# Kernel optimization log

Measured on AMD Instinct MI355X. Metric: run time of the kernel, lower is better.

## Reference

```python
import jax, jax.numpy as jnp
import numpy as np

B, S, D, H = 2, 2048, 2048, 32
HD = D // H  # head_dim = 64
NEG = -1e10


def setup_inputs() -> dict:
    key = jax.random.key(0)
    k1, k2, k3 = jax.random.split(key, 3)
    hidden_states = jax.random.normal(k1, (B, S, D), dtype=jnp.float32)
    W = jax.random.normal(k2, (D, 3 * D), dtype=jnp.float32) * (1.0 / np.sqrt(D))
    b = jax.random.normal(k3, (3 * D,), dtype=jnp.float32) * 0.02
    return {"hidden_states": hidden_states, "W": W, "b": b}


def reference(hidden_states, W, b):
    # fused QKV projection: [B,S,D] @ [D,3D] -> [B,S,3D]
    qvk = hidden_states @ W + b
    # OPT interleaved layout: reshape to [B,S,D,3]; channel 0=q, 1=v, 2=k
    qvk = qvk.reshape(B, S, D, 3)
    q = qvk[..., 0].reshape(B, S, H, HD)
    v = qvk[..., 1].reshape(B, S, H, HD)
    k = qvk[..., 2].reshape(B, S, H, HD)
    # causal bias: -1e10 strictly above diagonal, shape [1,1,S,S]
    bias = jnp.triu(jnp.full((S, S), NEG, dtype=jnp.float32), 1)[None, None]
    # dot_product_attention_weights: scale q by 1/sqrt(head_dim)
    scale = jnp.asarray(1.0 / np.sqrt(HD), dtype=jnp.float32)
    scores = jnp.einsum('bqhd,bkhd->bhqk', q * scale, k) + bias  # [B,H,S,S]
    attn_weights = jax.nn.softmax(scores, axis=-1)
    attn_output = jnp.einsum('bhqk,bkhd->bqhd', attn_weights, v)  # [B,S,H,HD]
    return attn_output.reshape(B, S, D)
```

## Files before the change

### kernel.cpp

```cpp
#include <hip/hip_runtime.h>
#include <hip/hip_bf16.h>
#include <stdint.h>

typedef unsigned short ushort_t;
typedef __bf16 bf16x8 __attribute__((ext_vector_type(8)));
typedef float f32x4 __attribute__((ext_vector_type(4)));
typedef float f32x16 __attribute__((ext_vector_type(16)));
typedef int int4v __attribute__((ext_vector_type(4)));
typedef ushort_t ushort8 __attribute__((ext_vector_type(8)));

__device__ __forceinline__ ushort_t f2bf(float f) {
  union { float f; unsigned int u; } v; v.f = f;
  unsigned int r = v.u + 0x7fffu + ((v.u >> 16) & 1u);
  return (ushort_t)(r >> 16);
}

__device__ __forceinline__ bf16x8 ld_bf8(const ushort_t* p) {
  return *reinterpret_cast<const bf16x8*>(p);
}

__device__ __forceinline__ void g2lds16(const void* g, void* l) {
  __builtin_amdgcn_global_load_lds(
      (const __attribute__((address_space(1))) unsigned int*)g,
      (__attribute__((address_space(3))) unsigned int*)l,
      16, 0, 0);
}

__device__ __forceinline__ float ex2(float x) { return __builtin_amdgcn_exp2f(x); }

__device__ __forceinline__ int cvtpk(float a, float b) {
  int r;
  asm("v_cvt_pk_bf16_f32 %0, %1, %2" : "=v"(r) : "v"(a), "v"(b));
  return r;
}

__global__ __launch_bounds__(256) void prep(const float* __restrict__ hs,
                                            ushort_t* __restrict__ Abf,
                                            const float* __restrict__ Win,
                                            ushort_t* __restrict__ Wt) {
  __shared__ ushort_t T[64][65];
  const int bid = blockIdx.x;
  const int t = threadIdx.x;
  if (bid < 4096) {
    int i = (bid * 256 + t) * 8;
    float4 a = *reinterpret_cast<const float4*>(hs + i);
    float4 b = *reinterpret_cast<const float4*>(hs + i + 4);
    ushort8 r;
    r[0] = f2bf(a.x); r[1] = f2bf(a.y); r[2] = f2bf(a.z); r[3] = f2bf(a.w);
    r[4] = f2bf(b.x); r[5] = f2bf(b.y); r[6] = f2bf(b.z); r[7] = f2bf(b.w);
    *reinterpret_cast<ushort8*>(Abf + i) = r;
  } else {
    const int tb = bid - 4096;
    const int k0 = (tb & 31) * 64;
    const int n0 = (tb >> 5) * 64;
#pragma unroll
    for (int i = 0; i < 16; ++i) {
      int idx = i * 256 + t;
      int r = idx >> 6, c = idx & 63;
      T[r][c] = f2bf(Win[(k0 + r) * 6144 + n0 + c]);
    }
    __syncthreads();
#pragma unroll
    for (int i = 0; i < 16; ++i) {
      int idx = i * 256 + t;
      int nr = idx >> 6, kc = idx & 63;
      Wt[(n0 + nr) * 2048 + k0 + kc] = T[kc][nr];
    }
  }
}

__global__ __launch_bounds__(256, 2) void gemm_qkv(
    const ushort_t* __restrict__ A, const ushort_t* __restrict__ Bt,
    const float* __restrict__ bias,
    ushort_t* __restrict__ Qb, ushort_t* __restrict__ Kb,
    ushort_t* __restrict__ VT) {
  __shared__ __align__(16) char smem[81920];
  ushort_t* A0 = (ushort_t*)smem;
  ushort_t* A1 = (ushort_t*)(smem + 16384);
  ushort_t* B0 = (ushort_t*)(smem + 32768);
  ushort_t* B1 = (ushort_t*)(smem + 57344);
  ushort_t* Cs = (ushort_t*)smem;
  const int t = threadIdx.x;
  const int w = t >> 6, l = t & 63;
  const int lo = l & 15, hi = l >> 4;
  const int wr = w >> 1, wc = w & 1;

  int bid = blockIdx.x;
  int swz = (bid & 7) * 128 + (bid >> 3);
  const int mt = swz & 31, nt = swz >> 5;
  const int bm = mt * 128;
  const int bn = nt * 192;

  f32x4 acc[4][6];
#pragma unroll
  for (int i = 0; i < 4; ++i)
#pragma unroll
    for (int j = 0; j < 6; ++j) acc[i][j] = f32x4{0.f, 0.f, 0.f, 0.f};

  const ushort_t* Ag = A + (size_t)bm * 2048;
  const ushort_t* Bg = Bt + (size_t)bn * 2048;

#define STAGE(Ad, Bd, kk_)                                            \
  do {                                                                \
    for (int r4 = 0; r4 < 4; ++r4) {                                  \
      int c_ = r4 * 256 + t;                                          \
      int row_ = c_ >> 3, s8_ = c_ & 7;                               \
      int half_ = s8_ >> 2, s4_ = s8_ & 3;                            \
      int slot_ = s4_ ^ ((row_ & 3) ^ ((row_ >> 2) & 3));             \
      g2lds16(Ag + row_ * 2048 + (kk_) + half_ * 32 + slot_ * 8,      \
              (Ad) + c_ * 8);                                         \
    }                                                                 \
    for (int r6 = 0; r6 < 6; ++r6) {                                  \
      int c_ = r6 * 256 + t;                                          \
      int row_ = c_ >> 3, s8_ = c_ & 7;                               \
      int half_ = s8_ >> 2, s4_ = s8_ & 3;                            \
      int slot_ = s4_ ^ ((row_ & 3) ^ ((row_ >> 2) & 3));             \
      g2lds16(Bg + row_ * 2048 + (kk_) + half_ * 32 + slot_ * 8,      \
              (Bd) + c_ * 8);                                         \
    }                                                                 \
  } while (0)

  STAGE(A0, B0, 0);
  __syncthreads();
  ushort_t *Ac = A0, *Bc = B0, *An = A1, *Bn = B1;

  for (int kk = 0; kk < 2048; kk += 64) {
    if (kk + 64 < 2048) STAGE(An, Bn, kk + 64);
#pragma unroll
    for (int ko = 0; ko < 64; ko += 32) {
      bf16x8 af[4], bfr[6];
#pragma unroll
      for (int mf = 0; mf < 4; ++mf) {
        int row = wr * 64 + mf * 16 + lo;
        int fr = (row & 3) ^ ((row >> 2) & 3);
        af[mf] = ld_bf8(Ac + row * 64 + ko + ((hi ^ fr) << 3));
      }
#pragma unroll
      for (int nf = 0; nf < 6; ++nf) {
        int row = wc * 96 + nf * 16 + lo;
        int fr = (row & 3) ^ ((row >> 2) & 3);
        bfr[nf] = ld_bf8(Bc + row * 64 + ko + ((hi ^ fr) << 3));
      }
      __builtin_amdgcn_s_setprio(1);
#pragma unroll
      for (int mf = 0; mf < 4; ++mf)
#pragma unroll
        for (int nf = 0; nf < 6; ++nf)
          acc[mf][nf] = __builtin_amdgcn_mfma_f32_16x16x32_bf16(
              af[mf], bfr[nf], acc[mf][nf], 0, 0, 0);
      __builtin_amdgcn_s_setprio(0);
    }
    __syncthreads();
    ushort_t* tmp;
    tmp = Ac; Ac = An; An = tmp;
    tmp = Bc; Bc = Bn; Bn = tmp;
  }
#undef STAGE

  float bv[6];
  int ch[6];
#pragma unroll
  for (int nf = 0; nf < 6; ++nf) {
    int nl = wc * 96 + nf * 16 + lo;
    bv[nf] = bias[bn + nl];
    ch[nf] = nl % 3;
  }
  const int b_ = bm >> 11;
  const int bh = (b_ << 5) + nt;
  const float QS = 0.125f * 1.44269504f;

#pragma unroll
  for (int h = 0; h < 2; ++h) {
    if (wr == h) {
#pragma unroll
      for (int mf = 0; mf < 4; ++mf)
#pragma unroll
        for (int nf = 0; nf < 6; ++nf) {
          int rloc = mf * 16 + hi * 4;
          int nl = wc * 96 + nf * 16 + lo;
          f32x4 a = acc[mf][nf];
#pragma unroll
          for (int j = 0; j < 4; ++j) {
            float v = a[j] + bv[nf];
            if (ch[nf] == 0) v *= QS;
            Cs[(rloc + j) * 200 + nl] = f2bf(v);
          }
        }
    }
    __syncthreads();
    const int sbase = (bm & 2047) + h * 64;
#pragma unroll
    for (int it = 0; it < 2; ++it) {
      int slot = it * 256 + t;
      int r = slot >> 3, g = slot & 7;
      ushort8 vq, vk;
#pragma unroll
      for (int u = 0; u < 8; ++u) {
        int hd = g * 8 + u;
        vq[u] = Cs[r * 200 + hd * 3];
        vk[u] = Cs[r * 200 + hd * 3 + 2];
      }
      size_t rowoff = ((size_t)bh * 2048 + sbase + r) * 64 + g * 8;
      *reinterpret_cast<ushort8*>(Qb + rowoff) = vq;
      *reinterpret_cast<ushort8*>(Kb + rowoff) = vk;
    }
#pragma unroll
    for (int it = 0; it < 2; ++it) {
      int slot = it * 256 + t;
      int hd = slot >> 3, sg = slot & 7;
      ushort8 vv;
#pragma unroll
      for (int u = 0; u < 8; ++u) vv[u] = Cs[(sg * 8 + u) * 200 + hd * 3 + 1];
      *reinterpret_cast<ushort8*>(VT + ((size_t)bh * 64 + hd) * 2048 + sbase +
                                  sg * 8) = vv;
    }
    __syncthreads();
  }
}

__device__ __forceinline__ void ldkv(const ushort_t* kp, const ushort_t* vp,
                                     bf16x8 k[4], bf16x8 v0[2], bf16x8 v1[2]) {
#pragma unroll
  for (int dc = 0; dc < 4; ++dc) k[dc] = ld_bf8(kp + dc * 16);
#pragma unroll
  for (int s = 0; s < 2; ++s) {
    v0[s] = ld_bf8(vp + s * 16);
    v1[s] = ld_bf8(vp + s * 16 + 32 * 2048);
  }
}

__device__ __forceinline__ void proc_chunk(const bf16x8 kf[4],
                                           const bf16x8 vf0[2],
                                           const bf16x8 vf1[2],
                                           const bf16x8 qf[4], f32x16& o0,
                                           f32x16& o1, float& mr, float& lr,
                                           bool diag, int ql, int hi) {
  f32x16 p;
#pragma unroll
  for (int r = 0; r < 16; ++r) p[r] = 0.f;
  __builtin_amdgcn_s_setprio(1);
#pragma unroll
  for (int dc = 0; dc < 4; ++dc)
    p = __builtin_amdgcn_mfma_f32_32x32x16_bf16(kf[dc], qf[dc], p, 0, 0, 0);
  __builtin_amdgcn_s_setprio(0);
  if (diag) {
#pragma unroll
    for (int r = 0; r < 16; ++r) {
      int kvr = (r & 3) + 8 * (r >> 2) + 4 * hi;
      if (kvr > ql) p[r] = -1e30f;
    }
  }
  float a0 = fmaxf(p[0], p[1]), a1 = fmaxf(p[2], p[3]);
  float a2 = fmaxf(p[4], p[5]), a3 = fmaxf(p[6], p[7]);
  float a4 = fmaxf(p[8], p[9]), a5 = fmaxf(p[10], p[11]);
  float a6 = fmaxf(p[12], p[13]), a7 = fmaxf(p[14], p[15]);
  float mx = fmaxf(fmaxf(fmaxf(a0, a1), fmaxf(a2, a3)),
                   fmaxf(fmaxf(a4, a5), fmaxf(a6, a7)));
  if (__any(mx > mr + 10.0f)) {
    mx = fmaxf(mx, __shfl_xor(mx, 32));
    float mn = fmaxf(mr, mx);
    float scl = ex2(mr - mn);
    mr = mn;
    lr *= scl;
#pragma unroll
    for (int r = 0; r < 16; ++r) { o0[r] *= scl; o1[r] *= scl; }
  }
#pragma unroll
  for (int r = 0; r < 16; ++r) p[r] = ex2(p[r] - mr);
  float s0 = (p[0] + p[1]) + (p[2] + p[3]);
  float s1 = (p[4] + p[5]) + (p[6] + p[7]);
  float s2 = (p[8] + p[9]) + (p[10] + p[11]);
  float s3 = (p[12] + p[13]) + (p[14] + p[15]);
  lr += (s0 + s1) + (s2 + s3);

  __builtin_amdgcn_s_setprio(1);
#pragma unroll
  for (int s = 0; s < 2; ++s) {
    int x0 = cvtpk(p[8 * s + 0], p[8 * s + 1]);
    int x1 = cvtpk(p[8 * s + 2], p[8 * s + 3]);
    int y0 = cvtpk(p[8 * s + 4], p[8 * s + 5]);
    int y1 = cvtpk(p[8 * s + 6], p[8 * s + 7]);
    int ox0 = __shfl_xor(x0, 32);
    int ox1 = __shfl_xor(x1, 32);
    int oy0 = __shfl_xor(y0, 32);
    int oy1 = __shfl_xor(y1, 32);
    int4v wv;
    wv[0] = hi ? oy0 : x0;
    wv[1] = hi ? oy1 : x1;
    wv[2] = hi ? y0 : ox0;
    wv[3] = hi ? y1 : ox1;
    bf16x8 pf = __builtin_bit_cast(bf16x8, wv);
    o0 = __builtin_amdgcn_mfma_f32_32x32x16_bf16(vf0[s], pf, o0, 0, 0, 0);
    o1 = __builtin_amdgcn_mfma_f32_32x32x16_bf16(vf1[s], pf, o1, 0, 0, 0);
  }
  __builtin_amdgcn_s_setprio(0);
}

__global__ __launch_bounds__(64) void attn(
    const ushort_t* __restrict__ Qb, const ushort_t* __restrict__ Kb,
    const ushort_t* __restrict__ VT, float* __restrict__ out) {
  __shared__ float Ld[32 * 66];
  const int l = threadIdx.x;
  const int ql = l & 31, hi = l >> 5;

  const int bid = blockIdx.x;
  const int bh = bid & 63;
  const int p = bid >> 6;
  const int nchB = 64 - p;
  const int q0A = p * 32;
  const int q0B = (63 - p) * 32;
  const int b_ = bh >> 5, h = bh & 31;

  const ushort_t* kbase = Kb + bh * 2048 * 64 + hi * 8;
  const ushort_t* vbase = VT + (bh * 64 + ql) * 2048 + hi * 8;
  const int KSTR = 32 * 64;
  const int VSTR = 32;

  bf16x8 qfA[4], qfB[4];
  {
    const ushort_t* qpA = Qb + (bh * 2048 + q0A + ql) * 64 + hi * 8;
    const ushort_t* qpB = Qb + (bh * 2048 + q0B + ql) * 64 + hi * 8;
#pragma unroll
    for (int dc = 0; dc < 4; ++dc) {
      qfA[dc] = ld_bf8(qpA + dc * 16);
      qfB[dc] = ld_bf8(qpB + dc * 16);
    }
  }

  f32x16 oA0, oA1, oB0, oB1;
#pragma unroll
  for (int r = 0; r < 16; ++r) {
    oA0[r] = 0.f; oA1[r] = 0.f; oB0[r] = 0.f; oB1[r] = 0.f;
  }
  float mA = -1e30f, lA = 0.f, mB = -1e30f, lB = 0.f;

  bf16x8 kX[4], vX0[2], vX1[2], kY[4], vY0[2], vY1[2];
  const ushort_t* kp = kbase + ql * 64;
  const ushort_t* vp = vbase;
  ldkv(kp, vp, kX, vX0, vX1);

  int c = 0;
  while (c + 2 <= nchB) {
    kp += KSTR; vp += VSTR;
    ldkv(kp, vp, kY, vY0, vY1);
    proc_chunk(kX, vX0, vX1, qfB, oB0, oB1, mB, lB, false, ql, hi);
    if (c <= p)
      proc_chunk(kX, vX0, vX1, qfA, oA0, oA1, mA, lA, (c == p), ql, hi);
    if (c + 2 < nchB) {
      kp += KSTR; vp += VSTR;
      ldkv(kp, vp, kX, vX0, vX1);
    }
    proc_chunk(kY, vY0, vY1, qfB, oB0, oB1, mB, lB, (c + 1 == nchB - 1), ql,
               hi);
    if (c + 1 <= p)
      proc_chunk(kY, vY0, vY1, qfA, oA0, oA1, mA, lA, (c + 1 == p), ql, hi);
    c += 2;
  }
  if (c < nchB) {
    proc_chunk(kX, vX0, vX1, qfB, oB0, oB1, mB, lB, true, ql, hi);
    if (c <= p)
      proc_chunk(kX, vX0, vX1, qfA, oA0, oA1, mA, lA, (c == p), ql, hi);
  }

#pragma unroll 1
  for (int tile = 0; tile < 2; ++tile) {
    const float lr = tile ? lB : lA;
    const float lrf = lr + __shfl_xor(lr, 32);
    const float inv = 1.0f / lrf;
    const int q0 = tile ? q0B : q0A;
#pragma unroll
    for (int r = 0; r < 16; ++r) {
      int hdv = (r & 3) + 8 * (r >> 2) + 4 * hi;
      Ld[ql * 66 + hdv] = (tile ? oB0[r] : oA0[r]) * inv;
      Ld[ql * 66 + 32 + hdv] = (tile ? oB1[r] : oA1[r]) * inv;
    }
    __syncthreads();
    float* op = out + (size_t)(b_ * 2048 + q0) * 2048 + h * 64 + l;
#pragma unroll
    for (int i = 0; i < 32; ++i) {
      op[(size_t)i * 2048] = Ld[i * 66 + l];
    }
    __syncthreads();
  }
}

extern "C" void kernel_launch(void* const* d_in, const int* in_sizes, int n_in,
                              void* d_out, int out_size, void* d_ws,
                              size_t ws_size, hipStream_t stream) {
  (void)in_sizes; (void)n_in; (void)out_size; (void)ws_size;
  const float* hs = (const float*)d_in[0];
  const float* W = (const float*)d_in[1];
  const float* bias = (const float*)d_in[2];
  float* out = (float*)d_out;

  char* ws = (char*)d_ws;
  ushort_t* Abf = (ushort_t*)(ws);
  ushort_t* Wt = (ushort_t*)(ws + (16u << 20));
  ushort_t* Qb = (ushort_t*)(ws + (40u << 20));
  ushort_t* Kb = (ushort_t*)(ws + (56u << 20));
  ushort_t* VT = (ushort_t*)(ws + (72u << 20));

  hipLaunchKernelGGL(prep, dim3(7168), dim3(256), 0, stream, hs, Abf, W, Wt);
  hipLaunchKernelGGL(gemm_qkv, dim3(1024), dim3(256), 0, stream, Abf, Wt, bias,
                     Qb, Kb, VT);
  hipLaunchKernelGGL(attn, dim3(2048), dim3(64), 0, stream, Qb, Kb, VT, out);
}
```

Before: 234.7 us.

## Split KV chunks across two waves per block with LDS softmax merge

The attention kernel now runs two wavefronts per block. Each wave processes alternating KV chunks (even or odd) for the same pair of query tiles, and the partial outputs, row maxima and sums are merged through shared memory with a log-sum-exp combine before the store. This halves the serial KV loop length per wave and adds parallelism. In exchange it costs extra LDS traffic, two more barriers and exp evaluations in the epilogue, plus duplicated Q register loads per wave.

```diff
diff --git a/kernel.cpp b/kernel.cpp
--- a/kernel.cpp
+++ b/kernel.cpp
@@ -296,11 +296,15 @@
   __builtin_amdgcn_s_setprio(0);
 }
 
-__global__ __launch_bounds__(64) void attn(
+__global__ __launch_bounds__(128) void attn(
     const ushort_t* __restrict__ Qb, const ushort_t* __restrict__ Kb,
     const ushort_t* __restrict__ VT, float* __restrict__ out) {
-  __shared__ float Ld[32 * 66];
-  const int l = threadIdx.x;
+  __shared__ float LO[2][32 * 66];
+  __shared__ float Lm[2][32];
+  __shared__ float Ll[2][32];
+  const int t = threadIdx.x;
+  const int wv = t >> 6;
+  const int l = t & 63;
   const int ql = l & 31, hi = l >> 5;
 
   const int bid = blockIdx.x;
@@ -313,8 +317,8 @@
 
   const ushort_t* kbase = Kb + bh * 2048 * 64 + hi * 8;
   const ushort_t* vbase = VT + (bh * 64 + ql) * 2048 + hi * 8;
-  const int KSTR = 32 * 64;
-  const int VSTR = 32;
+  const int KSTR2 = 2 * 32 * 64;
+  const int VSTR2 = 2 * 32;
 
   bf16x8 qfA[4], qfB[4];
   {
@@ -334,53 +338,88 @@
   }
   float mA = -1e30f, lA = 0.f, mB = -1e30f, lB = 0.f;
 
+  const int cnt = (nchB > wv) ? ((nchB - wv + 1) >> 1) : 0;
   bf16x8 kX[4], vX0[2], vX1[2], kY[4], vY0[2], vY1[2];
-  const ushort_t* kp = kbase + ql * 64;
-  const ushort_t* vp = vbase;
-  ldkv(kp, vp, kX, vX0, vX1);
-
-  int c = 0;
-  while (c + 2 <= nchB) {
-    kp += KSTR; vp += VSTR;
+  const ushort_t* kp = kbase + (wv * 32 + ql) * 64;
+  const ushort_t* vp = vbase + wv * 32;
+  if (cnt > 0) ldkv(kp, vp, kX, vX0, vX1);
+
+  int i = 0, c = wv;
+  while (i + 2 <= cnt) {
+    kp += KSTR2; vp += VSTR2;
     ldkv(kp, vp, kY, vY0, vY1);
-    proc_chunk(kX, vX0, vX1, qfB, oB0, oB1, mB, lB, false, ql, hi);
+    proc_chunk(kX, vX0, vX1, qfB, oB0, oB1, mB, lB, (c == nchB - 1), ql, hi);
     if (c <= p)
       proc_chunk(kX, vX0, vX1, qfA, oA0, oA1, mA, lA, (c == p), ql, hi);
-    if (c + 2 < nchB) {
-      kp += KSTR; vp += VSTR;
+    if (i + 2 < cnt) {
+      kp += KSTR2; vp += VSTR2;
       ldkv(kp, vp, kX, vX0, vX1);
     }
-    proc_chunk(kY, vY0, vY1, qfB, oB0, oB1, mB, lB, (c + 1 == nchB - 1), ql,
+    proc_chunk(kY, vY0, vY1, qfB, oB0, oB1, mB, lB, (c + 2 == nchB - 1), ql,
                hi);
-    if (c + 1 <= p)
-      proc_chunk(kY, vY0, vY1, qfA, oA0, oA1, mA, lA, (c + 1 == p), ql, hi);
-    c += 2;
-  }
-  if (c < nchB) {
-    proc_chunk(kX, vX0, vX1, qfB, oB0, oB1, mB, lB, true, ql, hi);
+    if (c + 2 <= p)
+      proc_chunk(kY, vY0, vY1, qfA, oA0, oA1, mA, lA, (c + 2 == p), ql, hi);
+    i += 2;
+    c += 4;
+  }
+  if (i < cnt) {
+    proc_chunk(kX, vX0, vX1, qfB, oB0, oB1, mB, lB, (c == nchB - 1), ql, hi);
     if (c <= p)
       proc_chunk(kX, vX0, vX1, qfA, oA0, oA1, mA, lA, (c == p), ql, hi);
   }
 
-#pragma unroll 1
-  for (int tile = 0; tile < 2; ++tile) {
-    const float lr = tile ? lB : lA;
-    const float lrf = lr + __shfl_xor(lr, 32);
-    const float inv = 1.0f / lrf;
-    const int q0 = tile ? q0B : q0A;
-#pragma unroll
-    for (int r = 0; r < 16; ++r) {
-      int hdv = (r & 3) + 8 * (r >> 2) + 4 * hi;
-      Ld[ql * 66 + hdv] = (tile ? oB0[r] : oA0[r]) * inv;
-      Ld[ql * 66 + 32 + hdv] = (tile ? oB1[r] : oA1[r]) * inv;
-    }
-    __syncthreads();
-    float* op = out + (size_t)(b_ * 2048 + q0) * 2048 + h * 64 + l;
-#pragma unroll
-    for (int i = 0; i < 32; ++i) {
-      op[(size_t)i * 2048] = Ld[i * 66 + l];
-    }
-    __syncthreads();
+  const float lrfA = lA + __shfl_xor(lA, 32);
+  const float lrfB = lB + __shfl_xor(lB, 32);
+
+#pragma unroll
+  for (int r = 0; r < 16; ++r) {
+    int hdv = (r & 3) + 8 * (r >> 2) + 4 * hi;
+    LO[wv][ql * 66 + hdv] = oA0[r];
+    LO[wv][ql * 66 + 32 + hdv] = oA1[r];
+  }
+  if (hi == 0) {
+    Lm[wv][ql] = mA;
+    Ll[wv][ql] = lrfA;
+  }
+  __syncthreads();
+  {
+    float* op = out + (size_t)(b_ * 2048 + q0A) * 2048 + h * 64 + l;
+#pragma unroll
+    for (int j = 0; j < 16; ++j) {
+      int q = wv * 16 + j;
+      float m0 = Lm[0][q], m1 = Lm[1][q];
+      float M = fmaxf(m0, m1);
+      float w0 = ex2(m0 - M), w1 = ex2(m1 - M);
+      float ls = w0 * Ll[0][q] + w1 * Ll[1][q];
+      float val = (w0 * LO[0][q * 66 + l] + w1 * LO[1][q * 66 + l]) / ls;
+      op[(size_t)q * 2048] = val;
+    }
+  }
+  __syncthreads();
+
+#pragma unroll
+  for (int r = 0; r < 16; ++r) {
+    int hdv = (r & 3) + 8 * (r >> 2) + 4 * hi;
+    LO[wv][ql * 66 + hdv] = oB0[r];
+    LO[wv][ql * 66 + 32 + hdv] = oB1[r];
+  }
+  if (hi == 0) {
+    Lm[wv][ql] = mB;
+    Ll[wv][ql] = lrfB;
+  }
+  __syncthreads();
+  {
+    float* op = out + (size_t)(b_ * 2048 + q0B) * 2048 + h * 64 + l;
+#pragma unroll
+    for (int j = 0; j < 16; ++j) {
+      int q = wv * 16 + j;
+      float m0 = Lm[0][q], m1 = Lm[1][q];
+      float M = fmaxf(m0, m1);
+      float w0 = ex2(m0 - M), w1 = ex2(m1 - M);
+      float ls = w0 * Ll[0][q] + w1 * Ll[1][q];
+      float val = (w0 * LO[0][q * 66 + l] + w1 * LO[1][q * 66 + l]) / ls;
+      op[(size_t)q * 2048] = val;
+    }
   }
 }
 
@@ -403,5 +442,5 @@
   hipLaunchKernelGGL(prep, dim3(7168), dim3(256), 0, stream, hs, Abf, W, Wt);
   hipLaunchKernelGGL(gemm_qkv, dim3(1024), dim3(256), 0, stream, Abf, Wt, bias,
                      Qb, Kb, VT);
-  hipLaunchKernelGGL(attn, dim3(2048), dim3(64), 0, stream, Qb, Kb, VT, out);
-}
+  hipLaunchKernelGGL(attn, dim3(2048), dim3(128), 0, stream, Qb, Kb, VT, out);
+}
```

Measured after the change: 250.0 us. +6.5%, slower.
